# Performance work log

Measured on AMD Instinct MI355X. Metric: run time of the kernel, lower is better.

## Reference

```python
import jax, jax.numpy as jnp
import numpy as np

B, S, I, H, O, F = 8192, 100, 15, 128, 2, 30  # batch, seq, input, hidden, out, future


def _lstm_cell(x, h, c, w_ih, w_hh, b):
    # PyTorch gate order: input, forget, cell(g), output
    gates = x @ w_ih.T + h @ w_hh.T + b  # [B, 4H]
    i, f, g, o = jnp.split(gates, 4, axis=-1)
    c2 = jax.nn.sigmoid(f) * c + jax.nn.sigmoid(i) * jnp.tanh(g)
    h2 = jax.nn.sigmoid(o) * jnp.tanh(c2)
    return h2, c2


def setup_inputs() -> dict:
    key = jax.random.key(0)
    ks = jax.random.split(key, 12)
    s = 1.0 / np.sqrt(H)  # PyTorch LSTM/Linear init scale
    u = lambda k, shape: jax.random.uniform(k, shape, jnp.float32, -s, s)
    return {
        "x": jax.random.normal(ks[0], (B, S, I), jnp.float32),
        "w_ih0": u(ks[1], (4 * H, I)),
        "w_hh0": u(ks[2], (4 * H, H)),
        "b_ih0": u(ks[3], (4 * H,)),
        "b_hh0": u(ks[4], (4 * H,)),
        "w_ih1": u(ks[5], (4 * H, H)),
        "w_hh1": u(ks[6], (4 * H, H)),
        "b_ih1": u(ks[7], (4 * H,)),
        "b_hh1": u(ks[8], (4 * H,)),
        "fc_w": u(ks[9], (O, H)),
        "fc_b": u(ks[10], (O,)),
        "future_frames": F,
    }


def reference(x, w_ih0, w_hh0, b_ih0, b_hh0, w_ih1, w_hh1, b_ih1, b_hh1, fc_w, fc_b, future_frames):
    bsz = x.shape[0]
    hid = w_hh0.shape[1]
    b0 = b_ih0 + b_hh0
    b1 = b_ih1 + b_hh1

    # ---- encoder: run full 2-layer LSTM over the observed sequence ----
    xs = jnp.transpose(x, (1, 0, 2))  # [S, B, I]
    z = jnp.zeros((bsz, hid), x.dtype)

    def enc_step(carry, xt):
        h0, c0, h1, c1 = carry
        h0, c0 = _lstm_cell(xt, h0, c0, w_ih0, w_hh0, b0)
        h1, c1 = _lstm_cell(h0, h1, c1, w_ih1, w_hh1, b1)
        return (h0, c0, h1, c1), None

    (h0, c0, h1, c1), _ = jax.lax.scan(enc_step, (z, z, z, z), xs)

    def dec_step(carry, _):
        h0, c0, h1, c1, inp = carry
        h0, c0 = _lstm_cell(inp, h0, c0, w_ih0, w_hh0, b0)
        h1, c1 = _lstm_cell(h0, h1, c1, w_ih1, w_hh1, b1)
        pred = h1 @ fc_w.T + fc_b  # [B, 2]
        nxt = inp.at[:, :2].set(pred)
        return (h0, c0, h1, c1, nxt), pred

    _, preds = jax.lax.scan(dec_step, (h0, c0, h1, c1, x[:, -1, :]), None, length=future_frames)
    return jnp.transpose(preds, (1, 0, 2))  # [B, future_frames, 2]
```

## Files before the change

### kernel.cpp

```cpp
#include <hip/hip_runtime.h>


typedef _Float16 half_t;
typedef _Float16 half8 __attribute__((ext_vector_type(8)));
typedef _Float16 half4 __attribute__((ext_vector_type(4)));
typedef float f32x4 __attribute__((ext_vector_type(4)));

#define SEQ 100
#define FUT 30
#define TOT (SEQ + FUT)
#define NIN 15
#define MB  16
#define CH  8
#define L2E 1.44269504f

#define MFMA32(A, B, C) __builtin_amdgcn_mfma_f32_16x16x32_f16((A), (B), (C), 0, 0, 0)
#define MFMA16(A, B, C) __builtin_amdgcn_mfma_f32_16x16x16f16((A), (B), (C), 0, 0, 0)

__global__ void prep_kernel(const float* __restrict__ w_ih0, const float* __restrict__ w_hh0,
                            const float* __restrict__ b_ih0, const float* __restrict__ b_hh0,
                            const float* __restrict__ w_ih1, const float* __restrict__ w_hh1,
                            const float* __restrict__ b_ih1, const float* __restrict__ b_hh1,
                            half_t* __restrict__ wsh)
{
  int idx = blockIdx.x * 256 + threadIdx.x;
  if (idx < 131072) {
    int seg = idx >> 16;
    int r   = idx & 65535;
    int n   = r >> 7, k = r & 127;
    int g   = (n >> 4) & 3;
    int row = g * 128 + ((n >> 6) << 4) + (n & 15);
    float sc = (g == 2) ? (2.0f * L2E) : (-L2E);
    const float* src = (seg == 0) ? w_hh0 : w_ih1;
    wsh[idx] = (half_t)(src[row * 128 + k] * sc);
  } else if (idx < 196608) {
    int r   = idx - 131072;
    int c   = r >> 12;
    int rem = r & 4095;
    int n   = rem >> 3, e = rem & 7;
    int k   = c * 8 + e;
    int g   = (n >> 4) & 3;
    int row = g * 128 + ((n >> 6) << 4) + (n & 15);
    float sc = (g == 2) ? (2.0f * L2E) : (-L2E);
    wsh[idx] = (half_t)(w_hh1[row * 128 + k] * sc);
  } else if (idx < 204800) {
    int r   = idx - 196608;
    int n   = r >> 4, k = r & 15;
    int g   = (n >> 4) & 3;
    int row = g * 128 + ((n >> 6) << 4) + (n & 15);
    float sc = (g == 2) ? (2.0f * L2E) : (-L2E);
    wsh[idx] = (half_t)((k < NIN) ? (w_ih0[row * NIN + k] * sc) : 0.0f);
  } else if (idx < 205824) {
    int r     = idx - 204800;
    float* bv = (float*)(wsh + 204800);
    int which = r >> 9, n = r & 511;
    int g     = (n >> 4) & 3;
    int row   = g * 128 + ((n >> 6) << 4) + (n & 15);
    float sc  = (g == 2) ? (2.0f * L2E) : (-L2E);
    bv[r] = ((which == 0) ? (b_ih0[row] + b_hh0[row]) : (b_ih1[row] + b_hh1[row])) * sc;
  }
}

__global__ __launch_bounds__(512, 2)
void lstm_kernel(const float* __restrict__ x,
                 const half_t* __restrict__ wsh,
                 const float* __restrict__ fcw,
                 const float* __restrict__ fcb,
                 float* __restrict__ out)
{
  __shared__ __align__(16) half_t swh1[65536];
  __shared__ __align__(16) half_t sh0[2][MB * 128];
  __shared__ __align__(16) half_t sh1[2][MB * 128];
  __shared__ __align__(16) half_t sxc[2][CH * 256];
  __shared__ __align__(16) half_t sdec[4 * MB * 4];
  __shared__ __align__(16) float  sbias[1024];
  __shared__ __align__(16) float  sfc[258];

  const half_t* WH0 = wsh;
  const half_t* WI1 = wsh + 65536;
  const half_t* WH1L = wsh + 131072;
  const half_t* WX  = wsh + 196608;
  const float*  BV  = (const float*)(wsh + 204800);

  const int tid   = threadIdx.x;
  const int wave  = tid >> 6;
  const int lane  = tid & 63;
  const int l16   = lane & 15;
  const int quad  = lane >> 4;
  const int nb    = wave * 64;
  const int bbase = blockIdx.x * MB;

  half8 wh0[4][4], wi1[4][4];
  #pragma unroll
  for (int kt = 0; kt < 4; ++kt) {
    #pragma unroll
    for (int g = 0; g < 4; ++g) {
      int n = nb + g * 16 + l16;
      int k = kt * 32 + quad * 8;
      wh0[kt][g] = *(const half8*)&WH0[n * 128 + k];
      wi1[kt][g] = *(const half8*)&WI1[n * 128 + k];
    }
  }
  half4 wxr[4];
  #pragma unroll
  for (int g = 0; g < 4; ++g)
    wxr[g] = *(const half4*)&WX[(nb + g * 16 + l16) * 16 + quad * 4];

  for (int it = tid; it < 8192; it += 512)
    ((uint4*)swh1)[it] = ((const uint4*)WH1L)[it];
  for (int it = tid; it < 1024; it += 512) sbias[it] = BV[it];
  if (tid < 256) sfc[tid] = fcw[tid];
  if (tid < 2)   sfc[256 + tid] = fcb[tid];
  {
    int b = (tid >> 4) & 15, i = tid & 15;
    float v = (i < NIN) ? x[(size_t)(bbase + b) * (SEQ * NIN) + 99 * NIN + i] : 0.f;
    sdec[(i >> 2) * 64 + b * 4 + (i & 3)] = (half_t)v;
  }
  {
    int e0 = tid * 4;
    int t  = e0 >> 8;
    int rm = e0 & 255;
    int qd = rm >> 6, b = (rm & 63) >> 2;
    half4 v;
    #pragma unroll
    for (int i = 0; i < 4; ++i) {
      int f = qd * 4 + i;
      v[i] = (f < NIN) ? (half_t)x[(size_t)(bbase + b) * (SEQ * NIN) + t * NIN + f]
                       : (half_t)0;
    }
    *(half4*)&sxc[0][t * 256 + qd * 64 + b * 4] = v;
  }
  for (int it = tid; it < MB * 128; it += 512) {
    sh0[0][it] = (half_t)0; sh0[1][it] = (half_t)0;
    sh1[0][it] = (half_t)0; sh1[1][it] = (half_t)0;
  }
  __syncthreads();

  float c0[4] = {0.f, 0.f, 0.f, 0.f};
  float c1[4] = {0.f, 0.f, 0.f, 0.f};
  const int kc = wave * 2 + (l16 >> 3);

  #define ACT_STORE(ACC, CS, DST)                                              \
    _Pragma("unroll")                                                          \
    for (int r = 0; r < 4; ++r) {                                              \
      float A  = __builtin_amdgcn_exp2f((ACC)[0][r]);                          \
      float C  = __builtin_amdgcn_exp2f((ACC)[1][r]);                          \
      float B  = __builtin_amdgcn_exp2f((ACC)[2][r]);                          \
      float D  = __builtin_amdgcn_exp2f((ACC)[3][r]);                          \
      float oA = 1.f + A, oB = 1.f + B, oC = 1.f + C, oD = 1.f + D;            \
      float P  = oA * oB;                                                      \
      float t  = (B - 1.f) * oC;                                               \
      float nm = fmaf((CS)[r], P, t);                                          \
      float rc = __builtin_amdgcn_rcpf(P * oC);                                \
      float cn = nm * rc;                                                      \
      (CS)[r] = cn;                                                            \
      float E  = __builtin_amdgcn_exp2f(2.0f * L2E * cn);                      \
      float h  = (E - 1.f) * __builtin_amdgcn_rcpf(oD * (1.f + E));            \
      int   m  = quad * 4 + r;                                                 \
      (DST)[m * 128 + ((kc ^ (m & 7)) << 3) + (l16 & 7)] = (half_t)h;          \
    }

  {
    f32x4 acc0[4];
    #pragma unroll
    for (int g = 0; g < 4; ++g) {
      float b = sbias[nb + g * 16 + l16];
      acc0[g] = (f32x4){b, b, b, b};
    }
    half4 ax = *(const half4*)&sxc[0][quad * 64 + l16 * 4];
    #pragma unroll
    for (int g = 0; g < 4; ++g) acc0[g] = MFMA16(ax, wxr[g], acc0[g]);
    ACT_STORE(acc0, c0, sh0[1])
  }
  __syncthreads();

  int cur = 0;
  for (int s = 0; s < TOT - 1; ++s) {
    const int nxt = cur ^ 1;

    if (s < SEQ && (s & (CH - 1)) == 0) {
      int q1 = (s >> 3) + 1;
      if (q1 * CH < SEQ) {
        int e0 = tid * 4;
        int t  = e0 >> 8;
        int rm = e0 & 255;
        int qd = rm >> 6, b = (rm & 63) >> 2;
        int j  = q1 * CH + t;
        half4 v;
        #pragma unroll
        for (int i = 0; i < 4; ++i) {
          int f = qd * 4 + i;
          v[i] = (f < NIN && j < SEQ)
                   ? (half_t)x[(size_t)(bbase + b) * (SEQ * NIN) + j * NIN + f]
                   : (half_t)0;
        }
        *(half4*)&sxc[q1 & 1][t * 256 + qd * 64 + b * 4] = v;
      }
    }

    f32x4 acc1[4], acc0[4];
    #pragma unroll
    for (int g = 0; g < 4; ++g) {
      float b1v = sbias[512 + nb + g * 16 + l16];
      float b0v = sbias[nb + g * 16 + l16];
      acc1[g] = (f32x4){b1v, b1v, b1v, b1v};
      acc0[g] = (f32x4){b0v, b0v, b0v, b0v};
    }
    #pragma unroll
    for (int kt = 0; kt < 4; ++kt) {
      int c  = kt * 4 + quad;
      int sw = ((c ^ (l16 & 7)) << 3);
      half8 a0 = *(const half8*)&sh0[nxt][l16 * 128 + sw];
      #pragma unroll
      for (int g = 0; g < 4; ++g) acc1[g] = MFMA32(a0, wi1[kt][g], acc1[g]);
      #pragma unroll
      for (int g = 0; g < 4; ++g) acc0[g] = MFMA32(a0, wh0[kt][g], acc0[g]);
      half8 a1 = *(const half8*)&sh1[cur][l16 * 128 + sw];
      #pragma unroll
      for (int g = 0; g < 4; ++g) {
        half8 bw = *(const half8*)&swh1[(c * 512 + nb + g * 16 + l16) * 8];
        acc1[g] = MFMA32(a1, bw, acc1[g]);
      }
    }
    if (s < SEQ) {
      half4 ax;
      if (s + 1 < SEQ) {
        int j = s + 1;
        ax = *(const half4*)&sxc[(j >> 3) & 1][(j & (CH - 1)) * 256 + quad * 64 + l16 * 4];
      } else {
        ax = *(const half4*)&sdec[quad * 64 + l16 * 4];
      }
      #pragma unroll
      for (int g = 0; g < 4; ++g) acc0[g] = MFMA16(ax, wxr[g], acc0[g]);
    }

    ACT_STORE(acc1, c1, sh1[nxt])

    if (s >= SEQ) {
      __syncthreads();
      if (tid < 256) {
        int b   = wave * 4 + (lane >> 4);
        int o   = (lane >> 3) & 1;
        int seg = lane & 7;
        float p = 0.f;
        #pragma unroll
        for (int cc = 0; cc < 2; ++cc) {
          int c = seg * 2 + cc;
          half8 hv = *(const half8*)&sh1[nxt][b * 128 + ((c ^ (b & 7)) << 3)];
          f32x4 w0 = *(const f32x4*)&sfc[o * 128 + c * 8];
          f32x4 w1 = *(const f32x4*)&sfc[o * 128 + c * 8 + 4];
          #pragma unroll
          for (int u = 0; u < 4; ++u) p = fmaf((float)hv[u], w0[u], p);
          #pragma unroll
          for (int u = 0; u < 4; ++u) p = fmaf((float)hv[4 + u], w1[u], p);
        }
        p += __shfl_down(p, 4);
        p += __shfl_down(p, 2);
        p += __shfl_down(p, 1);
        if (seg == 0) {
          p += sfc[256 + o];
          out[(size_t)(bbase + b) * (FUT * 2) + (s - SEQ) * 2 + o] = p;
          sdec[b * 4 + o] = (half_t)p;
        }
      }
      __syncthreads();
      half4 ax = *(const half4*)&sdec[quad * 64 + l16 * 4];
      #pragma unroll
      for (int g = 0; g < 4; ++g) acc0[g] = MFMA16(ax, wxr[g], acc0[g]);
    }

    ACT_STORE(acc0, c0, sh0[cur])
    __syncthreads();
    cur = nxt;
  }

  {
    const int nxt = cur ^ 1;
    f32x4 acc1[4];
    #pragma unroll
    for (int g = 0; g < 4; ++g) {
      float b = sbias[512 + nb + g * 16 + l16];
      acc1[g] = (f32x4){b, b, b, b};
    }
    #pragma unroll
    for (int kt = 0; kt < 4; ++kt) {
      int c  = kt * 4 + quad;
      int sw = ((c ^ (l16 & 7)) << 3);
      half8 a0 = *(const half8*)&sh0[nxt][l16 * 128 + sw];
      #pragma unroll
      for (int g = 0; g < 4; ++g) acc1[g] = MFMA32(a0, wi1[kt][g], acc1[g]);
      half8 a1 = *(const half8*)&sh1[cur][l16 * 128 + sw];
      #pragma unroll
      for (int g = 0; g < 4; ++g) {
        half8 bw = *(const half8*)&swh1[(c * 512 + nb + g * 16 + l16) * 8];
        acc1[g] = MFMA32(a1, bw, acc1[g]);
      }
    }
    ACT_STORE(acc1, c1, sh1[nxt])
    __syncthreads();
    if (tid < 256) {
      int b   = wave * 4 + (lane >> 4);
      int o   = (lane >> 3) & 1;
      int seg = lane & 7;
      float p = 0.f;
      #pragma unroll
      for (int cc = 0; cc < 2; ++cc) {
        int c = seg * 2 + cc;
        half8 hv = *(const half8*)&sh1[nxt][b * 128 + ((c ^ (b & 7)) << 3)];
        f32x4 w0 = *(const f32x4*)&sfc[o * 128 + c * 8];
        f32x4 w1 = *(const f32x4*)&sfc[o * 128 + c * 8 + 4];
        #pragma unroll
        for (int u = 0; u < 4; ++u) p = fmaf((float)hv[u], w0[u], p);
        #pragma unroll
        for (int u = 0; u < 4; ++u) p = fmaf((float)hv[4 + u], w1[u], p);
      }
      p += __shfl_down(p, 4);
      p += __shfl_down(p, 2);
      p += __shfl_down(p, 1);
      if (seg == 0) {
        p += sfc[256 + o];
        out[(size_t)(bbase + b) * (FUT * 2) + (FUT - 1) * 2 + o] = p;
      }
    }
  }
}

extern "C" void kernel_launch(void* const* d_in, const int* in_sizes, int n_in,
                              void* d_out, int out_size, void* d_ws, size_t ws_size,
                              hipStream_t stream)
{
  (void)in_sizes; (void)n_in; (void)out_size; (void)ws_size;
  const float* x     = (const float*)d_in[0];
  const float* w_ih0 = (const float*)d_in[1];
  const float* w_hh0 = (const float*)d_in[2];
  const float* b_ih0 = (const float*)d_in[3];
  const float* b_hh0 = (const float*)d_in[4];
  const float* w_ih1 = (const float*)d_in[5];
  const float* w_hh1 = (const float*)d_in[6];
  const float* b_ih1 = (const float*)d_in[7];
  const float* b_hh1 = (const float*)d_in[8];
  const float* fcw   = (const float*)d_in[9];
  const float* fcb   = (const float*)d_in[10];
  float*  out = (float*)d_out;
  half_t* wsh = (half_t*)d_ws;

  prep_kernel<<<(205824 + 255) / 256, 256, 0, stream>>>(
      w_ih0, w_hh0, b_ih0, b_hh0, w_ih1, w_hh1, b_ih1, b_hh1, wsh);
  lstm_kernel<<<8192 / MB, 512, 0, stream>>>(x, wsh, fcw, fcb, out);
}
```

Baseline: 643.2 us.

## Process 32 batch rows per block with two MFMA tiles sharing weights

Doubles the batch tile per block from 16 to 32 rows, computed as two 16-row MFMA halves that reuse each loaded weight fragment (register and LDS). This halves the grid and amortizes the per-step weight reads and barriers over twice the rows. The chunked shared-memory staging of x is replaced by per-lane float4 global prefetch one step ahead, and sh1 becomes single-buffered with an extra barrier before its store. In exchange, register pressure roughly doubles for accumulators and cell state, which may cause spills or reduce occupancy, and each block's serial dependency chain now holds twice the work.

```diff
diff --git a/kernel.cpp b/kernel.cpp
--- a/kernel.cpp
+++ b/kernel.cpp
@@ -10,8 +10,7 @@
 #define FUT 30
 #define TOT (SEQ + FUT)
 #define NIN 15
-#define MB  16
-#define CH  8
+#define MB  32
 #define L2E 1.44269504f
 
 #define MFMA32(A, B, C) __builtin_amdgcn_mfma_f32_16x16x32_f16((A), (B), (C), 0, 0, 0)
@@ -61,6 +60,14 @@
   }
 }
 
+__device__ __forceinline__ half4 xfrag(float4 v, int quad) {
+  float a = (quad < 3) ? v.x : v.y;
+  float b = (quad < 3) ? v.y : v.z;
+  float c = (quad < 3) ? v.z : v.w;
+  float d = (quad < 3) ? v.w : 0.0f;
+  return (half4){(half_t)a, (half_t)b, (half_t)c, (half_t)d};
+}
+
 __global__ __launch_bounds__(512, 2)
 void lstm_kernel(const float* __restrict__ x,
                  const half_t* __restrict__ wsh,
@@ -70,17 +77,16 @@
 {
   __shared__ __align__(16) half_t swh1[65536];
   __shared__ __align__(16) half_t sh0[2][MB * 128];
-  __shared__ __align__(16) half_t sh1[2][MB * 128];
-  __shared__ __align__(16) half_t sxc[2][CH * 256];
+  __shared__ __align__(16) half_t sh1[MB * 128];
   __shared__ __align__(16) half_t sdec[4 * MB * 4];
   __shared__ __align__(16) float  sbias[1024];
   __shared__ __align__(16) float  sfc[258];
 
-  const half_t* WH0 = wsh;
-  const half_t* WI1 = wsh + 65536;
+  const half_t* WH0  = wsh;
+  const half_t* WI1  = wsh + 65536;
   const half_t* WH1L = wsh + 131072;
-  const half_t* WX  = wsh + 196608;
-  const float*  BV  = (const float*)(wsh + 204800);
+  const half_t* WX   = wsh + 196608;
+  const float*  BV   = (const float*)(wsh + 204800);
 
   const int tid   = threadIdx.x;
   const int wave  = tid >> 6;
@@ -112,35 +118,17 @@
   if (tid < 256) sfc[tid] = fcw[tid];
   if (tid < 2)   sfc[256 + tid] = fcb[tid];
   {
-    int b = (tid >> 4) & 15, i = tid & 15;
+    int b = tid >> 4, i = tid & 15;
     float v = (i < NIN) ? x[(size_t)(bbase + b) * (SEQ * NIN) + 99 * NIN + i] : 0.f;
-    sdec[(i >> 2) * 64 + b * 4 + (i & 3)] = (half_t)v;
-  }
-  {
-    int e0 = tid * 4;
-    int t  = e0 >> 8;
-    int rm = e0 & 255;
-    int qd = rm >> 6, b = (rm & 63) >> 2;
-    half4 v;
-    #pragma unroll
-    for (int i = 0; i < 4; ++i) {
-      int f = qd * 4 + i;
-      v[i] = (f < NIN) ? (half_t)x[(size_t)(bbase + b) * (SEQ * NIN) + t * NIN + f]
-                       : (half_t)0;
-    }
-    *(half4*)&sxc[0][t * 256 + qd * 64 + b * 4] = v;
-  }
-  for (int it = tid; it < MB * 128; it += 512) {
-    sh0[0][it] = (half_t)0; sh0[1][it] = (half_t)0;
-    sh1[0][it] = (half_t)0; sh1[1][it] = (half_t)0;
-  }
-  __syncthreads();
-
-  float c0[4] = {0.f, 0.f, 0.f, 0.f};
-  float c1[4] = {0.f, 0.f, 0.f, 0.f};
+    sdec[(i >> 2) * (MB * 4) + b * 4 + (i & 3)] = (half_t)v;
+  }
+  for (int it = tid; it < MB * 128; it += 512) sh1[it] = (half_t)0;
+
+  float c0A[4] = {0,0,0,0}, c0B[4] = {0,0,0,0};
+  float c1A[4] = {0,0,0,0}, c1B[4] = {0,0,0,0};
   const int kc = wave * 2 + (l16 >> 3);
 
-  #define ACT_STORE(ACC, CS, DST)                                              \
+  #define ACT_COMPUTE(ACC, CS, HV)                                             \
     _Pragma("unroll")                                                          \
     for (int r = 0; r < 4; ++r) {                                              \
       float A  = __builtin_amdgcn_exp2f((ACC)[0][r]);                          \
@@ -156,89 +144,146 @@
       (CS)[r] = cn;                                                            \
       float E  = __builtin_amdgcn_exp2f(2.0f * L2E * cn);                      \
       float h  = (E - 1.f) * __builtin_amdgcn_rcpf(oD * (1.f + E));            \
-      int   m  = quad * 4 + r;                                                 \
-      (DST)[m * 128 + ((kc ^ (m & 7)) << 3) + (l16 & 7)] = (half_t)h;          \
-    }
+      (HV)[r] = (half_t)h;                                                     \
+    }
+
+  #define STORE_H(HV, DST, ROWOFF)                                             \
+    _Pragma("unroll")                                                          \
+    for (int r = 0; r < 4; ++r) {                                              \
+      int m = quad * 4 + r;                                                    \
+      (DST)[(ROWOFF + m) * 128 + ((kc ^ (m & 7)) << 3) + (l16 & 7)] = (HV)[r]; \
+    }
+
+  const int koff = (quad < 3) ? quad * 4 : 11;
+  const float* xpA = x + (size_t)(bbase + l16) * (SEQ * NIN) + koff;
+  const float* xpB = xpA + (size_t)16 * (SEQ * NIN);
 
   {
-    f32x4 acc0[4];
+    float4 x0A = *(const float4*)xpA;
+    float4 x0B = *(const float4*)xpB;
+    half4 axA = xfrag(x0A, quad), axB = xfrag(x0B, quad);
+    f32x4 accA[4], accB[4];
     #pragma unroll
     for (int g = 0; g < 4; ++g) {
       float b = sbias[nb + g * 16 + l16];
-      acc0[g] = (f32x4){b, b, b, b};
-    }
-    half4 ax = *(const half4*)&sxc[0][quad * 64 + l16 * 4];
-    #pragma unroll
-    for (int g = 0; g < 4; ++g) acc0[g] = MFMA16(ax, wxr[g], acc0[g]);
-    ACT_STORE(acc0, c0, sh0[1])
-  }
+      accA[g] = (f32x4){b, b, b, b};
+      accB[g] = (f32x4){b, b, b, b};
+    }
+    #pragma unroll
+    for (int g = 0; g < 4; ++g) {
+      accA[g] = MFMA16(axA, wxr[g], accA[g]);
+      accB[g] = MFMA16(axB, wxr[g], accB[g]);
+    }
+    half4 hA, hB;
+    ACT_COMPUTE(accA, c0A, hA)
+    ACT_COMPUTE(accB, c0B, hB)
+    STORE_H(hA, sh0[0], 0)
+    STORE_H(hB, sh0[0], 16)
+  }
+  xpA += NIN; xpB += NIN;
+  float4 xfA = *(const float4*)xpA;
+  float4 xfB = *(const float4*)xpB;
   __syncthreads();
 
-  int cur = 0;
   for (int s = 0; s < TOT - 1; ++s) {
-    const int nxt = cur ^ 1;
-
-    if (s < SEQ && (s & (CH - 1)) == 0) {
-      int q1 = (s >> 3) + 1;
-      if (q1 * CH < SEQ) {
-        int e0 = tid * 4;
-        int t  = e0 >> 8;
-        int rm = e0 & 255;
-        int qd = rm >> 6, b = (rm & 63) >> 2;
-        int j  = q1 * CH + t;
-        half4 v;
-        #pragma unroll
-        for (int i = 0; i < 4; ++i) {
-          int f = qd * 4 + i;
-          v[i] = (f < NIN && j < SEQ)
-                   ? (half_t)x[(size_t)(bbase + b) * (SEQ * NIN) + j * NIN + f]
-                   : (half_t)0;
-        }
-        *(half4*)&sxc[q1 & 1][t * 256 + qd * 64 + b * 4] = v;
-      }
-    }
-
-    f32x4 acc1[4], acc0[4];
-    #pragma unroll
-    for (int g = 0; g < 4; ++g) {
-      float b1v = sbias[512 + nb + g * 16 + l16];
-      float b0v = sbias[nb + g * 16 + l16];
-      acc1[g] = (f32x4){b1v, b1v, b1v, b1v};
-      acc0[g] = (f32x4){b0v, b0v, b0v, b0v};
-    }
-    #pragma unroll
-    for (int kt = 0; kt < 4; ++kt) {
-      int c  = kt * 4 + quad;
-      int sw = ((c ^ (l16 & 7)) << 3);
-      half8 a0 = *(const half8*)&sh0[nxt][l16 * 128 + sw];
-      #pragma unroll
-      for (int g = 0; g < 4; ++g) acc1[g] = MFMA32(a0, wi1[kt][g], acc1[g]);
-      #pragma unroll
-      for (int g = 0; g < 4; ++g) acc0[g] = MFMA32(a0, wh0[kt][g], acc0[g]);
-      half8 a1 = *(const half8*)&sh1[cur][l16 * 128 + sw];
+    const int cur = s & 1, nxt = cur ^ 1;
+
+    half4 axA, axB;
+    if (s < SEQ) {
+      if (s + 1 < SEQ) { axA = xfrag(xfA, quad); axB = xfrag(xfB, quad); }
+      else {
+        axA = *(const half4*)&sdec[quad * (MB * 4) + l16 * 4];
+        axB = *(const half4*)&sdec[quad * (MB * 4) + (16 + l16) * 4];
+      }
+    }
+    if (s + 2 < SEQ) {
+      xpA += NIN; xpB += NIN;
+      xfA = *(const float4*)xpA;
+      xfB = *(const float4*)xpB;
+    }
+
+    f32x4 acc1A[4], acc1B[4];
+    #pragma unroll
+    for (int g = 0; g < 4; ++g) {
+      float b = sbias[512 + nb + g * 16 + l16];
+      acc1A[g] = (f32x4){b, b, b, b};
+      acc1B[g] = (f32x4){b, b, b, b};
+    }
+    #pragma unroll
+    for (int kt = 0; kt < 4; ++kt) {
+      int c  = kt * 4 + quad;
+      int sw = ((c ^ (l16 & 7)) << 3);
+      half8 a1A = *(const half8*)&sh1[l16 * 128 + sw];
+      half8 a1B = *(const half8*)&sh1[(16 + l16) * 128 + sw];
       #pragma unroll
       for (int g = 0; g < 4; ++g) {
         half8 bw = *(const half8*)&swh1[(c * 512 + nb + g * 16 + l16) * 8];
-        acc1[g] = MFMA32(a1, bw, acc1[g]);
-      }
+        acc1A[g] = MFMA32(a1A, bw, acc1A[g]);
+        acc1B[g] = MFMA32(a1B, bw, acc1B[g]);
+      }
+    }
+    #pragma unroll
+    for (int kt = 0; kt < 4; ++kt) {
+      int c  = kt * 4 + quad;
+      int sw = ((c ^ (l16 & 7)) << 3);
+      half8 a0A = *(const half8*)&sh0[cur][l16 * 128 + sw];
+      half8 a0B = *(const half8*)&sh0[cur][(16 + l16) * 128 + sw];
+      #pragma unroll
+      for (int g = 0; g < 4; ++g) {
+        acc1A[g] = MFMA32(a0A, wi1[kt][g], acc1A[g]);
+        acc1B[g] = MFMA32(a0B, wi1[kt][g], acc1B[g]);
+      }
+    }
+
+    f32x4 acc0A[4];
+    #pragma unroll
+    for (int g = 0; g < 4; ++g) {
+      float b = sbias[nb + g * 16 + l16];
+      acc0A[g] = (f32x4){b, b, b, b};
+    }
+    #pragma unroll
+    for (int kt = 0; kt < 4; ++kt) {
+      int c  = kt * 4 + quad;
+      int sw = ((c ^ (l16 & 7)) << 3);
+      half8 a0A = *(const half8*)&sh0[cur][l16 * 128 + sw];
+      #pragma unroll
+      for (int g = 0; g < 4; ++g) acc0A[g] = MFMA32(a0A, wh0[kt][g], acc0A[g]);
     }
     if (s < SEQ) {
-      half4 ax;
-      if (s + 1 < SEQ) {
-        int j = s + 1;
-        ax = *(const half4*)&sxc[(j >> 3) & 1][(j & (CH - 1)) * 256 + quad * 64 + l16 * 4];
-      } else {
-        ax = *(const half4*)&sdec[quad * 64 + l16 * 4];
-      }
-      #pragma unroll
-      for (int g = 0; g < 4; ++g) acc0[g] = MFMA16(ax, wxr[g], acc0[g]);
-    }
-
-    ACT_STORE(acc1, c1, sh1[nxt])
+      #pragma unroll
+      for (int g = 0; g < 4; ++g) acc0A[g] = MFMA16(axA, wxr[g], acc0A[g]);
+    }
+    half4 h1Av;
+    ACT_COMPUTE(acc1A, c1A, h1Av)
+
+    f32x4 acc0B[4];
+    #pragma unroll
+    for (int g = 0; g < 4; ++g) {
+      float b = sbias[nb + g * 16 + l16];
+      acc0B[g] = (f32x4){b, b, b, b};
+    }
+    #pragma unroll
+    for (int kt = 0; kt < 4; ++kt) {
+      int c  = kt * 4 + quad;
+      int sw = ((c ^ (l16 & 7)) << 3);
+      half8 a0B = *(const half8*)&sh0[cur][(16 + l16) * 128 + sw];
+      #pragma unroll
+      for (int g = 0; g < 4; ++g) acc0B[g] = MFMA32(a0B, wh0[kt][g], acc0B[g]);
+    }
+    if (s < SEQ) {
+      #pragma unroll
+      for (int g = 0; g < 4; ++g) acc0B[g] = MFMA16(axB, wxr[g], acc0B[g]);
+    }
+    half4 h1Bv;
+    ACT_COMPUTE(acc1B, c1B, h1Bv)
+
+    __syncthreads();
+    STORE_H(h1Av, sh1, 0)
+    STORE_H(h1Bv, sh1, 16)
 
     if (s >= SEQ) {
       __syncthreads();
-      if (tid < 256) {
+      {
         int b   = wave * 4 + (lane >> 4);
         int o   = (lane >> 3) & 1;
         int seg = lane & 7;
@@ -246,7 +291,7 @@
         #pragma unroll
         for (int cc = 0; cc < 2; ++cc) {
           int c = seg * 2 + cc;
-          half8 hv = *(const half8*)&sh1[nxt][b * 128 + ((c ^ (b & 7)) << 3)];
+          half8 hv = *(const half8*)&sh1[b * 128 + ((c ^ (b & 7)) << 3)];
           f32x4 w0 = *(const f32x4*)&sfc[o * 128 + c * 8];
           f32x4 w1 = *(const f32x4*)&sfc[o * 128 + c * 8 + 4];
           #pragma unroll
@@ -264,41 +309,67 @@
         }
       }
       __syncthreads();
-      half4 ax = *(const half4*)&sdec[quad * 64 + l16 * 4];
-      #pragma unroll
-      for (int g = 0; g < 4; ++g) acc0[g] = MFMA16(ax, wxr[g], acc0[g]);
-    }
-
-    ACT_STORE(acc0, c0, sh0[cur])
+      half4 dxA = *(const half4*)&sdec[quad * (MB * 4) + l16 * 4];
+      half4 dxB = *(const half4*)&sdec[quad * (MB * 4) + (16 + l16) * 4];
+      #pragma unroll
+      for (int g = 0; g < 4; ++g) {
+        acc0A[g] = MFMA16(dxA, wxr[g], acc0A[g]);
+        acc0B[g] = MFMA16(dxB, wxr[g], acc0B[g]);
+      }
+    }
+
+    {
+      half4 h0Av, h0Bv;
+      ACT_COMPUTE(acc0A, c0A, h0Av)
+      STORE_H(h0Av, sh0[nxt], 0)
+      ACT_COMPUTE(acc0B, c0B, h0Bv)
+      STORE_H(h0Bv, sh0[nxt], 16)
+    }
     __syncthreads();
-    cur = nxt;
   }
 
   {
-    const int nxt = cur ^ 1;
-    f32x4 acc1[4];
+    const int cur = (TOT - 1) & 1;
+    f32x4 acc1A[4], acc1B[4];
     #pragma unroll
     for (int g = 0; g < 4; ++g) {
       float b = sbias[512 + nb + g * 16 + l16];
-      acc1[g] = (f32x4){b, b, b, b};
-    }
-    #pragma unroll
-    for (int kt = 0; kt < 4; ++kt) {
-      int c  = kt * 4 + quad;
-      int sw = ((c ^ (l16 & 7)) << 3);
-      half8 a0 = *(const half8*)&sh0[nxt][l16 * 128 + sw];
-      #pragma unroll
-      for (int g = 0; g < 4; ++g) acc1[g] = MFMA32(a0, wi1[kt][g], acc1[g]);
-      half8 a1 = *(const half8*)&sh1[cur][l16 * 128 + sw];
+      acc1A[g] = (f32x4){b, b, b, b};
+      acc1B[g] = (f32x4){b, b, b, b};
+    }
+    #pragma unroll
+    for (int kt = 0; kt < 4; ++kt) {
+      int c  = kt * 4 + quad;
+      int sw = ((c ^ (l16 & 7)) << 3);
+      half8 a1A = *(const half8*)&sh1[l16 * 128 + sw];
+      half8 a1B = *(const half8*)&sh1[(16 + l16) * 128 + sw];
       #pragma unroll
       for (int g = 0; g < 4; ++g) {
         half8 bw = *(const half8*)&swh1[(c * 512 + nb + g * 16 + l16) * 8];
-        acc1[g] = MFMA32(a1, bw, acc1[g]);
-      }
-    }
-    ACT_STORE(acc1, c1, sh1[nxt])
+        acc1A[g] = MFMA32(a1A, bw, acc1A[g]);
+        acc1B[g] = MFMA32(a1B, bw, acc1B[g]);
+      }
+    }
+    #pragma unroll
+    for (int kt = 0; kt < 4; ++kt) {
+      int c  = kt * 4 + quad;
+      int sw = ((c ^ (l16 & 7)) << 3);
+      half8 a0A = *(const half8*)&sh0[cur][l16 * 128 + sw];
+      half8 a0B = *(const half8*)&sh0[cur][(16 + l16) * 128 + sw];
+      #pragma unroll
+      for (int g = 0; g < 4; ++g) {
+        acc1A[g] = MFMA32(a0A, wi1[kt][g], acc1A[g]);
+        acc1B[g] = MFMA32(a0B, wi1[kt][g], acc1B[g]);
+      }
+    }
+    half4 h1Av, h1Bv;
+    ACT_COMPUTE(acc1A, c1A, h1Av)
+    ACT_COMPUTE(acc1B, c1B, h1Bv)
     __syncthreads();
-    if (tid < 256) {
+    STORE_H(h1Av, sh1, 0)
+    STORE_H(h1Bv, sh1, 16)
+    __syncthreads();
+    {
       int b   = wave * 4 + (lane >> 4);
       int o   = (lane >> 3) & 1;
       int seg = lane & 7;
@@ -306,7 +377,7 @@
       #pragma unroll
       for (int cc = 0; cc < 2; ++cc) {
         int c = seg * 2 + cc;
-        half8 hv = *(const half8*)&sh1[nxt][b * 128 + ((c ^ (b & 7)) << 3)];
+        half8 hv = *(const half8*)&sh1[b * 128 + ((c ^ (b & 7)) << 3)];
         f32x4 w0 = *(const f32x4*)&sfc[o * 128 + c * 8];
         f32x4 w1 = *(const f32x4*)&sfc[o * 128 + c * 8 + 4];
         #pragma unroll
```

Result: slower. 705.7 us (+9.7%).
